# Kernel optimization log

Measured on AMD Instinct MI355X. Metric: run time of the kernel, lower is better.

Reference implementation:

```python
import jax, jax.numpy as jnp
import numpy as np

B, IN_F, K_INT, OUT_F = 256, 512, 75, 64
INIT = 0.05


def setup_inputs() -> dict:
    key = jax.random.key(0)
    k_x, k_t = jax.random.split(key)
    x = jax.random.normal(k_x, (B, IN_F), dtype=jnp.float32)
    T = jax.random.normal(k_t, (IN_F, K_INT, OUT_F), dtype=jnp.float32) * INIT
    return {"x": x, "T": T}


def reference(x, T):
    # M: [B, K, O] = x @ T flattened over (K, O)
    Bn = x.shape[0]
    M = (x @ T.reshape(T.shape[0], -1)).reshape(Bn, T.shape[1], T.shape[2])
    # pairwise L1 distance over K: [B, B, O]
    # (original materializes [B, B, K, O] broadcasted diff; same math)
    M_diff = M[None, :, :, :] - M[:, None, :, :]
    distance = jnp.abs(M_diff).sum(axis=2)           # [B, B, O]
    exp_distance = jnp.exp(-distance)                # [B, B, O]
    minibatch_features = exp_distance.sum(axis=1) - 1.0  # [B, O]; -1 removes self-distance
    return minibatch_features
```

## Files before the change

### kernel.cpp

```cpp
#include <hip/hip_runtime.h>


typedef __attribute__((ext_vector_type(8))) short bf16x8;
typedef __attribute__((ext_vector_type(4))) float f32x4;
typedef unsigned short u16;
typedef unsigned int u32;

__device__ inline u16 f2bf(float f) {
  u32 u = __float_as_uint(f);
  return (u16)((u + 0x7FFFu + ((u >> 16) & 1u)) >> 16);
}
__device__ inline short bftrunc(float f) {
  return (short)(__float_as_uint(f) >> 16);
}
__device__ inline float bflo(u32 u) { return __uint_as_float(u << 16); }
__device__ inline float bfhi(u32 u) { return __uint_as_float(u & 0xFFFF0000u); }

__global__ __launch_bounds__(256) void md_gemm_direct(const float* __restrict__ x,
                                                      const float* __restrict__ T,
                                                      float* __restrict__ Mt2) {
  const int tid = threadIdx.x;
  const int l = tid & 63, w = tid >> 6;
  const int bx = blockIdx.x;
  const int b0 = (blockIdx.y << 6) + ((w & 1) << 5);
  const int z = blockIdx.z;
  const int lr = l & 15;
  const int ko = (l >> 4) << 3;
  const int oh = (w >> 1) << 5;

  const float* At = T + (z * 256 + ko) * 4800 + bx * 64 + oh + lr;
  const float* Bx0 = x + (b0 + lr) * 512 + z * 256 + ko;
  const float* Bx1 = Bx0 + 16 * 512;

  f32x4 d00 = {0.f, 0.f, 0.f, 0.f}, d01 = d00, d10 = d00, d11 = d00;

#pragma unroll 2
  for (int kk = 0; kk < 8; ++kk) {
    bf16x8 a0, a1, f0, f1;
    const float* Ak = At + (kk << 5) * 4800;
#pragma unroll
    for (int e = 0; e < 8; ++e) {
      a0[e] = bftrunc(Ak[e * 4800]);
      a1[e] = bftrunc(Ak[e * 4800 + 16]);
    }
    const float4 b00 = *reinterpret_cast<const float4*>(Bx0 + (kk << 5));
    const float4 b01 = *reinterpret_cast<const float4*>(Bx0 + (kk << 5) + 4);
    const float4 b10 = *reinterpret_cast<const float4*>(Bx1 + (kk << 5));
    const float4 b11 = *reinterpret_cast<const float4*>(Bx1 + (kk << 5) + 4);
    f0[0] = bftrunc(b00.x); f0[1] = bftrunc(b00.y); f0[2] = bftrunc(b00.z); f0[3] = bftrunc(b00.w);
    f0[4] = bftrunc(b01.x); f0[5] = bftrunc(b01.y); f0[6] = bftrunc(b01.z); f0[7] = bftrunc(b01.w);
    f1[0] = bftrunc(b10.x); f1[1] = bftrunc(b10.y); f1[2] = bftrunc(b10.z); f1[3] = bftrunc(b10.w);
    f1[4] = bftrunc(b11.x); f1[5] = bftrunc(b11.y); f1[6] = bftrunc(b11.z); f1[7] = bftrunc(b11.w);

    d00 = __builtin_amdgcn_mfma_f32_16x16x32_bf16(a0, f0, d00, 0, 0, 0);
    d01 = __builtin_amdgcn_mfma_f32_16x16x32_bf16(a0, f1, d01, 0, 0, 0);
    d10 = __builtin_amdgcn_mfma_f32_16x16x32_bf16(a1, f0, d10, 0, 0, 0);
    d11 = __builtin_amdgcn_mfma_f32_16x16x32_bf16(a1, f1, d11, 0, 0, 0);
  }

  float* Mt = Mt2 + z * 1228800;
  const int n0 = (bx << 6) + oh;
#pragma unroll
  for (int r = 0; r < 4; ++r) {
    const int row = ((l >> 4) << 2) + r;
    {
      const int n = n0 + row;
      float* base = Mt + (n & 63) * 19200 + (n >> 6) * 256;
      base[b0 + lr] = d00[r];
      base[b0 + 16 + lr] = d01[r];
    }
    {
      const int n = n0 + 16 + row;
      float* base = Mt + (n & 63) * 19200 + (n >> 6) * 256;
      base[b0 + lr] = d10[r];
      base[b0 + 16 + lr] = d11[r];
    }
  }
}

__global__ __launch_bounds__(512) void md_pair4(const float* __restrict__ Mt2,
                                                float* __restrict__ out) {
  const int bid = blockIdx.x;
  const int o = bid & 63;
  const int it = bid >> 6;
  const int ibase = it << 5;
  const int tid = threadIdx.x;
  const int is = tid & 15;
  const int jg = tid >> 4;

  __shared__ alignas(16) u16 MjB[38 * 256];
  __shared__ alignas(16) float MiF[38 * 32];

  const float* M0 = Mt2 + o * 19200;
  const float* M1 = M0 + 1228800;

  float d[2][8];
#pragma unroll
  for (int a = 0; a < 2; ++a)
#pragma unroll
    for (int b = 0; b < 8; ++b) d[a][b] = 0.0f;

  for (int h = 0; h < 2; ++h) {
    const int kbase = h * 38;
    __syncthreads();
    for (int idx = tid; idx < 38 * 64; idx += 512) {
      const int kk = idx >> 6, q = idx & 63;
      const int gk = kbase + kk;
      uint2 p;
      if (gk < 75) {
        const int goff = gk * 256 + (q << 2);
        const float4 v0 = *reinterpret_cast<const float4*>(M0 + goff);
        const float4 v1 = *reinterpret_cast<const float4*>(M1 + goff);
        p.x = (u32)f2bf(v0.x + v1.x) | ((u32)f2bf(v0.y + v1.y) << 16);
        p.y = (u32)f2bf(v0.z + v1.z) | ((u32)f2bf(v0.w + v1.w) << 16);
      } else {
        p = make_uint2(0u, 0u);
      }
      *reinterpret_cast<uint2*>(MjB + kk * 256 + (q << 2)) = p;
    }
    for (int idx = tid; idx < 38 * 32; idx += 512) {
      const int kk = idx >> 5, ii = idx & 31;
      const int gk = kbase + kk;
      const int goff = gk * 256 + ibase + ii;
      MiF[kk * 32 + ii] = (gk < 75) ? (M0[goff] + M1[goff]) : 0.0f;
    }
    __syncthreads();

#pragma unroll 19
    for (int kk = 0; kk < 38; ++kk) {
      const float2 vi = *reinterpret_cast<const float2*>(MiF + kk * 32 + (is << 1));
      const uint4 ju = *reinterpret_cast<const uint4*>(MjB + kk * 256 + (jg << 3));
      const float ja[8] = {bflo(ju.x), bfhi(ju.x), bflo(ju.y), bfhi(ju.y),
                           bflo(ju.z), bfhi(ju.z), bflo(ju.w), bfhi(ju.w)};
#pragma unroll
      for (int b = 0; b < 8; ++b) {
        d[0][b] += __builtin_fabsf(ja[b] - vi.x);
        d[1][b] += __builtin_fabsf(ja[b] - vi.y);
      }
    }
  }

  float s[2];
#pragma unroll
  for (int a = 0; a < 2; ++a) {
    const int ia = ibase + (is << 1) + a;
    float t = 0.0f;
#pragma unroll
    for (int b = 0; b < 8; ++b) {
      const int j = (jg << 3) + b;
      const float e = __expf(-d[a][b]);
      t += (j == ia) ? 0.0f : e;
    }
    s[a] = t;
  }

  __syncthreads();
  float* red = reinterpret_cast<float*>(MjB);
  red[((is << 1) + 0) * 33 + jg] = s[0];
  red[((is << 1) + 1) * 33 + jg] = s[1];
  __syncthreads();
  if (tid < 32) {
    float t = 0.0f;
#pragma unroll
    for (int g = 0; g < 32; ++g) t += red[tid * 33 + g];
    out[(ibase + tid) * 64 + o] = t;
  }
}

extern "C" void kernel_launch(void* const* d_in, const int* in_sizes, int n_in,
                              void* d_out, int out_size, void* d_ws, size_t ws_size,
                              hipStream_t stream) {
  const float* x = (const float*)d_in[0];
  const float* T = (const float*)d_in[1];
  float* out = (float*)d_out;

  float* Mt2 = (float*)d_ws;

  md_gemm_direct<<<dim3(75, 4, 2), 256, 0, stream>>>(x, T, Mt2);
  md_pair4<<<512, 512, 0, stream>>>(Mt2, out);
}
```

Baseline: 50.35 us.

## Exploit pairwise distance symmetry with upper-triangular tile pairs and atomic accumulation

The pairwise kernel now handles only the upper-triangular 64x64 (i,j) tile pairs, 10 per output channel, and reuses each computed exp(-distance) for both the row sum and the column sum. This roughly halves the L1-distance arithmetic. Both panels are stored as bf16 in shared memory covering all 75 K values, so the K loop no longer needs two halves. Partial sums go to the output through atomicAdd, which requires a memset beforehand. That adds an extra launch, atomic traffic and a second reduction pass on off-diagonal blocks.

Measured after the change: 50.15 us. Within noise of the previous version (-0.4%).

```diff
diff --git a/kernel.cpp b/kernel.cpp
--- a/kernel.cpp
+++ b/kernel.cpp
@@ -78,21 +78,50 @@
   }
 }
 
-__global__ __launch_bounds__(512) void md_pair4(const float* __restrict__ Mt2,
-                                                float* __restrict__ out) {
+#define PSTR 72
+__global__ __launch_bounds__(256) void md_pair_sym(const float* __restrict__ Mt2,
+                                                   float* __restrict__ out) {
   const int bid = blockIdx.x;
   const int o = bid & 63;
-  const int it = bid >> 6;
-  const int ibase = it << 5;
+  const int tp = bid >> 6;
+  const int TI[10] = {0, 0, 0, 0, 1, 1, 1, 2, 2, 3};
+  const int TJ[10] = {0, 1, 2, 3, 1, 2, 3, 2, 3, 3};
+  const int ti = TI[tp], tj = TJ[tp];
+  const bool diag = (ti == tj);
   const int tid = threadIdx.x;
-  const int is = tid & 15;
-  const int jg = tid >> 4;
 
-  __shared__ alignas(16) u16 MjB[38 * 256];
-  __shared__ alignas(16) float MiF[38 * 32];
+  __shared__ alignas(16) u16 panel[2][75 * PSTR];
+  u16* Mi = panel[0];
+  u16* Mj = diag ? panel[0] : panel[1];
 
   const float* M0 = Mt2 + o * 19200;
   const float* M1 = M0 + 1228800;
+
+  for (int idx = tid; idx < 1200; idx += 256) {
+    const int kk = idx >> 4, q = idx & 15;
+    {
+      const int goff = kk * 256 + (ti << 6) + (q << 2);
+      const float4 v0 = *reinterpret_cast<const float4*>(M0 + goff);
+      const float4 v1 = *reinterpret_cast<const float4*>(M1 + goff);
+      uint2 p;
+      p.x = (u32)f2bf(v0.x + v1.x) | ((u32)f2bf(v0.y + v1.y) << 16);
+      p.y = (u32)f2bf(v0.z + v1.z) | ((u32)f2bf(v0.w + v1.w) << 16);
+      *reinterpret_cast<uint2*>(Mi + kk * PSTR + (q << 2)) = p;
+    }
+    if (!diag) {
+      const int goff = kk * 256 + (tj << 6) + (q << 2);
+      const float4 v0 = *reinterpret_cast<const float4*>(M0 + goff);
+      const float4 v1 = *reinterpret_cast<const float4*>(M1 + goff);
+      uint2 p;
+      p.x = (u32)f2bf(v0.x + v1.x) | ((u32)f2bf(v0.y + v1.y) << 16);
+      p.y = (u32)f2bf(v0.z + v1.z) | ((u32)f2bf(v0.w + v1.w) << 16);
+      *reinterpret_cast<uint2*>(Mj + kk * PSTR + (q << 2)) = p;
+    }
+  }
+  __syncthreads();
+
+  const int is = tid & 31;
+  const int jg = tid >> 5;
 
   float d[2][8];
 #pragma unroll
@@ -100,70 +129,56 @@
 #pragma unroll
     for (int b = 0; b < 8; ++b) d[a][b] = 0.0f;
 
-  for (int h = 0; h < 2; ++h) {
-    const int kbase = h * 38;
-    __syncthreads();
-    for (int idx = tid; idx < 38 * 64; idx += 512) {
-      const int kk = idx >> 6, q = idx & 63;
-      const int gk = kbase + kk;
-      uint2 p;
-      if (gk < 75) {
-        const int goff = gk * 256 + (q << 2);
-        const float4 v0 = *reinterpret_cast<const float4*>(M0 + goff);
-        const float4 v1 = *reinterpret_cast<const float4*>(M1 + goff);
-        p.x = (u32)f2bf(v0.x + v1.x) | ((u32)f2bf(v0.y + v1.y) << 16);
-        p.y = (u32)f2bf(v0.z + v1.z) | ((u32)f2bf(v0.w + v1.w) << 16);
-      } else {
-        p = make_uint2(0u, 0u);
-      }
-      *reinterpret_cast<uint2*>(MjB + kk * 256 + (q << 2)) = p;
-    }
-    for (int idx = tid; idx < 38 * 32; idx += 512) {
-      const int kk = idx >> 5, ii = idx & 31;
-      const int gk = kbase + kk;
-      const int goff = gk * 256 + ibase + ii;
-      MiF[kk * 32 + ii] = (gk < 75) ? (M0[goff] + M1[goff]) : 0.0f;
-    }
-    __syncthreads();
-
-#pragma unroll 19
-    for (int kk = 0; kk < 38; ++kk) {
-      const float2 vi = *reinterpret_cast<const float2*>(MiF + kk * 32 + (is << 1));
-      const uint4 ju = *reinterpret_cast<const uint4*>(MjB + kk * 256 + (jg << 3));
-      const float ja[8] = {bflo(ju.x), bfhi(ju.x), bflo(ju.y), bfhi(ju.y),
-                           bflo(ju.z), bfhi(ju.z), bflo(ju.w), bfhi(ju.w)};
+#pragma unroll 15
+  for (int kk = 0; kk < 75; ++kk) {
+    const u32 vi = *reinterpret_cast<const u32*>(Mi + kk * PSTR + (is << 1));
+    const uint4 ju = *reinterpret_cast<const uint4*>(Mj + kk * PSTR + (jg << 3));
+    const float i0 = bflo(vi), i1 = bfhi(vi);
+    const float ja[8] = {bflo(ju.x), bfhi(ju.x), bflo(ju.y), bfhi(ju.y),
+                         bflo(ju.z), bfhi(ju.z), bflo(ju.w), bfhi(ju.w)};
 #pragma unroll
-      for (int b = 0; b < 8; ++b) {
-        d[0][b] += __builtin_fabsf(ja[b] - vi.x);
-        d[1][b] += __builtin_fabsf(ja[b] - vi.y);
-      }
+    for (int b = 0; b < 8; ++b) {
+      d[0][b] += __builtin_fabsf(ja[b] - i0);
+      d[1][b] += __builtin_fabsf(ja[b] - i1);
     }
   }
 
-  float s[2];
+  float isum[2] = {0.0f, 0.0f};
+  float jsum[8] = {0.f, 0.f, 0.f, 0.f, 0.f, 0.f, 0.f, 0.f};
 #pragma unroll
   for (int a = 0; a < 2; ++a) {
-    const int ia = ibase + (is << 1) + a;
-    float t = 0.0f;
+    const int gi = (ti << 6) + (is << 1) + a;
 #pragma unroll
     for (int b = 0; b < 8; ++b) {
-      const int j = (jg << 3) + b;
+      const int gj = (tj << 6) + (jg << 3) + b;
       const float e = __expf(-d[a][b]);
-      t += (j == ia) ? 0.0f : e;
+      if (gi != gj) { isum[a] += e; jsum[b] += e; }
     }
-    s[a] = t;
   }
 
   __syncthreads();
-  float* red = reinterpret_cast<float*>(MjB);
-  red[((is << 1) + 0) * 33 + jg] = s[0];
-  red[((is << 1) + 1) * 33 + jg] = s[1];
+  float* red = reinterpret_cast<float*>(panel);
+  red[((is << 1) + 0) * 33 + jg] = isum[0];
+  red[((is << 1) + 1) * 33 + jg] = isum[1];
   __syncthreads();
-  if (tid < 32) {
+  if (tid < 64) {
     float t = 0.0f;
 #pragma unroll
-    for (int g = 0; g < 32; ++g) t += red[tid * 33 + g];
-    out[(ibase + tid) * 64 + o] = t;
+    for (int g = 0; g < 8; ++g) t += red[tid * 33 + g];
+    atomicAdd(&out[((ti << 6) + tid) * 64 + o], t);
+  }
+
+  if (!diag) {
+    __syncthreads();
+#pragma unroll
+    for (int b = 0; b < 8; ++b) red[((jg << 3) + b) * 33 + is] = jsum[b];
+    __syncthreads();
+    if (tid < 64) {
+      float t = 0.0f;
+#pragma unroll
+      for (int g = 0; g < 32; ++g) t += red[tid * 33 + g];
+      atomicAdd(&out[((tj << 6) + tid) * 64 + o], t);
+    }
   }
 }
 
@@ -176,6 +191,7 @@
 
   float* Mt2 = (float*)d_ws;
 
+  hipMemsetAsync(out, 0, 256 * 64 * sizeof(float), stream);
   md_gemm_direct<<<dim3(75, 4, 2), 256, 0, stream>>>(x, T, Mt2);
-  md_pair4<<<512, 512, 0, stream>>>(Mt2, out);
+  md_pair_sym<<<640, 256, 0, stream>>>(Mt2, out);
 }
```
